# Kernel tuning notes

Hardware: AMD Instinct MI355X
Metric: run time of the kernel (lower is better)

Reference implementation:

```python
import jax, jax.numpy as jnp
import numpy as np

EPS = 1e-6


def _mp_match(reps, att, kernel):
    """BiMPM multi-perspective match.
    reps: (B,L,D); att: (B,L,D) or (B,1,D); kernel: (M,D).
    Returns (B,L,1+M): [tanh(sum(reps*att)), tanh(sum_d reps*kernel_m*att)].
    """
    prod = reps * att                                   # (B,L,D)
    cos = jnp.tanh(jnp.sum(prod, axis=-1, keepdims=True))   # (B,L,1)
    mp = jnp.tanh(jnp.einsum('bld,md->blm', prod, kernel))  # (B,L,M)
    return jnp.concatenate([cos, mp], axis=-1)


def setup_inputs() -> dict:
    key = jax.random.key(0)
    ks = jax.random.split(key, 12)
    B, Llt, Lrt, D, M, A = 32, 128, 128, 512, 64, 128
    H = D // 2
    u = lambda k, shape: jax.random.uniform(k, shape, jnp.float32, -0.05, 0.05)  # keras 'uniform' init
    return {
        'reps_lt': jax.random.normal(ks[0], (B, Llt, D), jnp.float32),
        'h_lt_fw': jax.random.normal(ks[1], (B, H), jnp.float32),
        'h_lt_bw': jax.random.normal(ks[2], (B, H), jnp.float32),
        'reps_rt': jax.random.normal(ks[3], (B, Lrt, D), jnp.float32),
        'h_rt_fw': jax.random.normal(ks[4], (B, H), jnp.float32),
        'h_rt_bw': jax.random.normal(ks[5], (B, H), jnp.float32),
        'kernel_full': u(ks[6], (M, D)),
        'kernel_mpool': u(ks[7], (M, D)),
        'attn_w1': u(ks[8], (D, A)),
        'diag_w': u(ks[9], (A,)),
        'kernel_att': u(ks[10], (M, D)),
        'kernel_maxatt': u(ks[11], (M, D)),
    }


def reference(reps_lt, h_lt_fw, h_lt_bw, reps_rt, h_rt_fw, h_rt_bw,
              kernel_full, kernel_mpool, attn_w1, diag_w,
              kernel_att, kernel_maxatt):
    # ---- full match: each left timestep vs last BiLSTM state of right ----
    h_rt = jnp.concatenate([h_rt_fw, h_rt_bw], axis=-1)[:, None, :]  # (B,1,D)
    full = _mp_match(reps_lt, h_rt, kernel_full)                     # (B,Ll,1+M)

    # ---- max-pooling match ----
    # t[b,r,l,m] = tanh(sum_d R[b,r,d]*K[m,d]*L[b,l,d]); max over right positions r
    r_scaled = jnp.einsum('brd,md->brmd', reps_rt, kernel_mpool)     # (B,Lr,M,D)
    t = jnp.tanh(jnp.einsum('brmd,bld->brlm', r_scaled, reps_lt))    # (B,Lr,Ll,M)
    mpool = jnp.max(t, axis=1)                                       # (B,Ll,M)

    # ---- attentive match ----
    a_lt = jnp.tanh(reps_lt @ attn_w1) * diag_w                      # (B,Ll,A)
    a_rt = jnp.tanh(reps_rt @ attn_w1)                               # (B,Lr,A)
    scores = jnp.einsum('bla,bra->blr', a_lt, a_rt)                  # (B,Ll,Lr)
    probs = jax.nn.softmax(scores, axis=-1)
    att = jnp.einsum('blr,brd->bld', probs, reps_rt)                 # (B,Ll,D)
    attentive = _mp_match(reps_lt, att, kernel_att)                  # (B,Ll,1+M)

    # ---- max-attentive match ----
    num = jnp.einsum('bld,brd->blr', reps_lt, reps_rt)
    n_lt = jnp.sqrt(jnp.maximum(jnp.sum(reps_lt * reps_lt, -1), EPS))[:, :, None]
    n_rt = jnp.sqrt(jnp.maximum(jnp.sum(reps_rt * reps_rt, -1), EPS))[:, None, :]
    rel = num / n_rt / n_lt                                          # (B,Ll,Lr)
    idx = jnp.argmax(rel, axis=2)                                    # (B,Ll) int
    max_att = jnp.take_along_axis(reps_rt, idx[:, :, None], axis=1)  # (B,Ll,D)
    maxatt = _mp_match(reps_lt, max_att, kernel_maxatt)              # (B,Ll,1+M)

    return jnp.concatenate([full, mpool, attentive, maxatt], axis=-1)  # (B,Ll,3+4M)
```

## Files before the change

kernel.cpp:

```cpp
#include <hip/hip_runtime.h>
#include <hip/hip_bf16.h>
#include <math.h>
#include <stdint.h>

typedef __attribute__((ext_vector_type(8))) short short8;
typedef __attribute__((ext_vector_type(4))) float float4v;

#define DEV static __device__ __forceinline__

DEV float bflo(unsigned int u) { union { unsigned int i; float f; } v; v.i = u << 16; return v.f; }
DEV float bfhi(unsigned int u) { union { unsigned int i; float f; } v; v.i = u & 0xffff0000u; return v.f; }
DEV unsigned short f2bf(float f) {
    union { float f; unsigned int i; } v; v.f = f;
    unsigned int x = v.i;
    return (unsigned short)((x + 0x7fffu + ((x >> 16) & 1u)) >> 16);
}
DEV unsigned int pack2(float a, float b) { return (unsigned int)f2bf(a) | ((unsigned int)f2bf(b) << 16); }
#if __has_builtin(__builtin_amdgcn_cvt_pk_bf16_f32)
DEV unsigned int pack2_fast(float a, float b) {
    typedef __attribute__((ext_vector_type(2))) short short2v;
    short2v r = __builtin_amdgcn_cvt_pk_bf16_f32(a, b);
    union { short2v s; unsigned int u; } v; v.s = r; return v.u;
}
#else
DEV unsigned int pack2_fast(float a, float b) { return pack2(a, b); }
#endif
DEV void unpack8(uint4 u, float* f) {
    f[0]=bflo(u.x); f[1]=bfhi(u.x); f[2]=bflo(u.y); f[3]=bfhi(u.y);
    f[4]=bflo(u.z); f[5]=bfhi(u.z); f[6]=bflo(u.w); f[7]=bfhi(u.w);
}

DEV void async16(const unsigned short* g, unsigned short* l) {
    __builtin_amdgcn_global_load_lds(
        (const __attribute__((address_space(1))) unsigned int*)g,
        (__attribute__((address_space(3))) unsigned int*)l, 16, 0, 0);
}

__global__ __launch_bounds__(256) void prep_kernel(const float* __restrict__ lt,
                                                   const float* __restrict__ rt,
                                                   const float* __restrict__ kf,
                                                   const float* __restrict__ kmp,
                                                   const float* __restrict__ ka,
                                                   const float* __restrict__ km,
                                                   const float* __restrict__ w1,
                                                   unsigned short* __restrict__ ltb,
                                                   unsigned short* __restrict__ rtb,
                                                   unsigned short* __restrict__ kb,
                                                   unsigned short* __restrict__ w1t,
                                                   unsigned short* __restrict__ rtbT,
                                                   double* __restrict__ rsq) {
    __shared__ double ws2[2][2];
    __shared__ float tile[32][33];
    int bid = blockIdx.x, t = threadIdx.x;
    if (bid < 1024) {
        bool isRt = bid >= 512;
        int base = (isRt ? (bid - 512) : bid) * 8;
        int rl = t >> 7;
        int c  = t & 127;
        const float* srcb = isRt ? rt : lt;
        unsigned short* dstb = isRt ? rtb : ltb;
        #pragma unroll
        for (int p = 0; p < 4; ++p) {
            int row = base + p * 2 + rl;
            const float* src = srcb + (size_t)row * 512;
            float4 v = *(const float4*)(src + c * 4);
            ushort4 o;
            o.x = f2bf(v.x); o.y = f2bf(v.y); o.z = f2bf(v.z); o.w = f2bf(v.w);
            *(ushort4*)(dstb + (size_t)row * 512 + c * 4) = o;
            if (isRt) {
                double s = (double)v.x * v.x + (double)v.y * v.y
                         + (double)v.z * v.z + (double)v.w * v.w;
                #pragma unroll
                for (int off = 1; off < 64; off <<= 1) s += __shfl_xor(s, off, 64);
                if ((c & 63) == 0) ws2[rl][c >> 6] = s;
                __syncthreads();
                if (c == 0) rsq[row] = 1.0 / sqrt(ws2[rl][0] + ws2[rl][1]);
                __syncthreads();
            }
        }
    } else if (bid < 1152) {
        int kbk = bid - 1024;
        int ksel = kbk >> 5;
        const float* src = (ksel == 0) ? kf : (ksel == 1) ? kmp : (ksel == 2) ? ka : km;
        int off = (kbk & 31) * 1024 + t * 4;
        float4 v = *(const float4*)(src + off);
        ushort4 o;
        o.x = f2bf(v.x); o.y = f2bf(v.y); o.z = f2bf(v.z); o.w = f2bf(v.w);
        *(ushort4*)(kb + ksel * 32768 + off) = o;
    } else if (bid < 1216) {
        int b2 = bid - 1152;
        int d0 = (b2 & 15) * 32, a0 = (b2 >> 4) * 32;
        int r = t >> 5, c = t & 31;
        #pragma unroll
        for (int i = 0; i < 32; i += 8)
            tile[r + i][c] = w1[(size_t)(d0 + r + i) * 128 + a0 + c];
        __syncthreads();
        #pragma unroll
        for (int i = 0; i < 32; i += 8)
            w1t[(size_t)(a0 + r + i) * 512 + d0 + c] = f2bf(tile[c][r + i]);
    } else {
        int b3 = bid - 1216;
        int b = b3 >> 6;
        int tid = b3 & 63;
        int d0 = (tid & 15) * 32;
        int r0 = (tid >> 4) * 32;
        int r = t >> 5, c = t & 31;
        #pragma unroll
        for (int i = 0; i < 32; i += 8)
            tile[r + i][c] = rt[(size_t)(b * 128 + r0 + r + i) * 512 + d0 + c];
        __syncthreads();
        #pragma unroll
        for (int i = 0; i < 32; i += 8)
            rtbT[(size_t)(b * 512 + d0 + r + i) * 128 + r0 + c] = f2bf(tile[c][r + i]);
    }
}

__global__ __launch_bounds__(256, 3) void uber_kernel(
        const unsigned short* __restrict__ ltb,
        const unsigned short* __restrict__ rtb,
        const unsigned short* __restrict__ kmb,
        const unsigned short* __restrict__ w1t,
        const float* __restrict__ diag,
        unsigned short* __restrict__ a_all,
        const double* __restrict__ rsq,
        unsigned int* __restrict__ candp,
        float* __restrict__ out) {
    __shared__ __align__(16) unsigned char smem[52224];
    int bx = blockIdx.x;
    int t = threadIdx.x;
    int wave = t >> 6, lane = t & 63;
    int q = lane >> 4, col = lane & 15, kq = q * 8;

    if (bx < 2048) {
        int xcd = bx & 7, jj = bx >> 3;
        int b = xcd * 4 + (jj >> 6);
        int m = jj & 63;
        unsigned short* ltS = (unsigned short*)smem;
        unsigned short* rtL = (unsigned short*)(smem + 16384);
        float (*mx)[2] = (float(*)[2])(smem + 16384 + 32768);
        int wl = wave & 1, wr = wave >> 1;
        const unsigned short* ltp = ltb + (size_t)b * 65536;
        const unsigned short* rtp = rtb + (size_t)b * 65536;
        const unsigned short* kr = kmb + (size_t)m * 512;
        int srow = t >> 3, cg8 = t & 7, cg = cg8 * 8;
        int gsw = (cg8 ^ (srow & 7)) * 8;
        int wbase = (t & ~63) * 8;

        #pragma unroll
        for (int it = 0; it < 4; ++it)
            async16(rtp + (size_t)(it * 32 + srow) * 512 + gsw,
                    rtL + it * 2048 + wbase);
        uint4 pk = *(const uint4*)(kr + cg);
        uint4 plt[4];
        #pragma unroll
        for (int it = 0; it < 4; ++it)
            plt[it] = *(const uint4*)(ltp + (size_t)(it * 32 + srow) * 512 + cg);

        float4v acc[4][4] = {};
        for (int k0i = 0; k0i < 8; ++k0i) {
            float kf8[8]; unpack8(pk, kf8);
            #pragma unroll
            for (int it = 0; it < 4; ++it) {
                int row = it * 32 + srow;
                float lf[8]; unpack8(plt[it], lf);
                uint4 s;
                s.x = pack2_fast(lf[0] * kf8[0], lf[1] * kf8[1]);
                s.y = pack2_fast(lf[2] * kf8[2], lf[3] * kf8[3]);
                s.z = pack2_fast(lf[4] * kf8[4], lf[5] * kf8[5]);
                s.w = pack2_fast(lf[6] * kf8[6], lf[7] * kf8[7]);
                *(uint4*)&ltS[row * 64 + gsw] = s;
            }
            __syncthreads();
            if (k0i < 7) {
                int k0n = (k0i + 1) * 64;
                int bofs = ((k0i + 1) & 1) * 8192;
                #pragma unroll
                for (int it = 0; it < 4; ++it)
                    async16(rtp + (size_t)(it * 32 + srow) * 512 + k0n + gsw,
                            rtL + bofs + it * 2048 + wbase);
                pk = *(const uint4*)(kr + k0n + cg);
                #pragma unroll
                for (int it = 0; it < 4; ++it)
                    plt[it] = *(const uint4*)(ltp + (size_t)(it * 32 + srow) * 512 + k0n + cg);
            }
            const unsigned short* rb = rtL + (k0i & 1) * 8192;
            #pragma unroll
            for (int kk = 0; kk < 64; kk += 32) {
                short8 af[4], bfr[4];
                #pragma unroll
                for (int i = 0; i < 4; ++i) {
                    int rowA = wl * 64 + i * 16 + col;
                    int slotA = ((kk >> 3) + q) ^ (rowA & 7);
                    af[i] = *(const short8*)&ltS[rowA * 64 + slotA * 8];
                }
                #pragma unroll
                for (int j = 0; j < 4; ++j) {
                    int row = wr * 64 + j * 16 + col;
                    int slot = ((kk >> 3) + q) ^ (row & 7);
                    bfr[j] = *(const short8*)&rb[row * 64 + slot * 8];
                }
                #pragma unroll
                for (int i = 0; i < 4; ++i)
                    #pragma unroll
                    for (int j = 0; j < 4; ++j)
                        acc[i][j] = __builtin_amdgcn_mfma_f32_16x16x32_bf16(af[i], bfr[j], acc[i][j], 0, 0, 0);
            }
            __syncthreads();
        }
        #pragma unroll
        for (int i = 0; i < 4; ++i)
            #pragma unroll
            for (int ii = 0; ii < 4; ++ii) {
                float v = fmaxf(fmaxf(acc[i][0][ii], acc[i][1][ii]), fmaxf(acc[i][2][ii], acc[i][3][ii]));
                #pragma unroll
                for (int off = 1; off < 16; off <<= 1) v = fmaxf(v, __shfl_xor(v, off, 64));
                if (col == 0) mx[wl * 64 + i * 16 + q * 4 + ii][wr] = v;
            }
        __syncthreads();
        if (t < 128)
            out[((size_t)(b * 128 + t)) * 259 + 65 + m] = tanhf(fmaxf(mx[t][0], mx[t][1]));

    } else if (bx < 2080) {
        int sb = bx - 2048;
        int xcd = sb & 7;
        int b = xcd * 4 + (sb >> 3);
        unsigned short* ltS = (unsigned short*)smem;
        unsigned short* rtL = (unsigned short*)(smem + 16384);
        float* rsqf = (float*)(smem + 49152);
        unsigned int (*candL)[2] = (unsigned int(*)[2])(smem + 49664);
        int wl = wave & 1, wr = wave >> 1;
        const unsigned short* ltp = ltb + (size_t)b * 65536;
        const unsigned short* rtp = rtb + (size_t)b * 65536;
        int srow = t >> 3, cg8 = t & 7, cg = cg8 * 8;
        int gsw = (cg8 ^ (srow & 7)) * 8;
        int wbase = (t & ~63) * 8;

        #pragma unroll
        for (int it = 0; it < 4; ++it)
            async16(rtp + (size_t)(it * 32 + srow) * 512 + gsw,
                    rtL + it * 2048 + wbase);
        uint4 plt[4];
        #pragma unroll
        for (int it = 0; it < 4; ++it)
            plt[it] = *(const uint4*)(ltp + (size_t)(it * 32 + srow) * 512 + cg);
        if (t < 128) rsqf[t] = (float)rsq[b * 128 + t];

        float4v acc[4][4] = {};
        for (int k0i = 0; k0i < 8; ++k0i) {
            #pragma unroll
            for (int it = 0; it < 4; ++it) {
                int row = it * 32 + srow;
                *(uint4*)&ltS[row * 64 + gsw] = plt[it];
            }
            __syncthreads();
            if (k0i < 7) {
                int k0n = (k0i + 1) * 64;
                int bofs = ((k0i + 1) & 1) * 8192;
                #pragma unroll
                for (int it = 0; it < 4; ++it)
                    async16(rtp + (size_t)(it * 32 + srow) * 512 + k0n + gsw,
                            rtL + bofs + it * 2048 + wbase);
                #pragma unroll
                for (int it = 0; it < 4; ++it)
                    plt[it] = *(const uint4*)(ltp + (size_t)(it * 32 + srow) * 512 + k0n + cg);
            }
            const unsigned short* rb = rtL + (k0i & 1) * 8192;
            #pragma unroll
            for (int kk = 0; kk < 64; kk += 32) {
                short8 af[4], bfr[4];
                #pragma unroll
                for (int i = 0; i < 4; ++i) {
                    int rowA = wl * 64 + i * 16 + col;
                    int slotA = ((kk >> 3) + q) ^ (rowA & 7);
                    af[i] = *(const short8*)&ltS[rowA * 64 + slotA * 8];
                }
                #pragma unroll
                for (int j = 0; j < 4; ++j) {
                    int row = wr * 64 + j * 16 + col;
                    int slot = ((kk >> 3) + q) ^ (row & 7);
                    bfr[j] = *(const short8*)&rb[row * 64 + slot * 8];
                }
                #pragma unroll
                for (int i = 0; i < 4; ++i)
                    #pragma unroll
                    for (int j = 0; j < 4; ++j)
                        acc[i][j] = __builtin_amdgcn_mfma_f32_16x16x32_bf16(af[i], bfr[j], acc[i][j], 0, 0, 0);
            }
            __syncthreads();
        }
        float rq[4];
        #pragma unroll
        for (int j = 0; j < 4; ++j) rq[j] = rsqf[wr * 64 + j * 16 + col];
        #pragma unroll
        for (int i = 0; i < 4; ++i)
            #pragma unroll
            for (int ii = 0; ii < 4; ++ii) {
                float v1 = -3.0e38f, v2 = -3.0e38f; int i1 = 0, i2 = 1;
                #pragma unroll
                for (int j = 0; j < 4; ++j) {
                    int rc = wr * 64 + j * 16 + col;
                    float s = acc[i][j][ii] * rq[j];
                    if (s > v1) { v2 = v1; i2 = i1; v1 = s; i1 = rc; }
                    else if (s > v2) { v2 = s; i2 = rc; }
                }
                #pragma unroll
                for (int off = 1; off < 16; off <<= 1) {
                    float u1 = __shfl_xor(v1, off, 64); int j1 = __shfl_xor(i1, off, 64);
                    float u2 = __shfl_xor(v2, off, 64); int j2 = __shfl_xor(i2, off, 64);
                    if (u1 > v1) {
                        float ov = v1; int oi = i1;
                        v1 = u1; i1 = j1;
                        if (u2 > ov) { v2 = u2; i2 = j2; } else { v2 = ov; i2 = oi; }
                    } else if (u1 > v2) { v2 = u1; i2 = j1; }
                }
                if (col == 0)
                    candL[wl * 64 + i * 16 + q * 4 + ii][wr] =
                        (unsigned int)i1 | ((unsigned int)i2 << 8);
            }
        __syncthreads();
        if (t < 128)
            candp[b * 128 + t] = candL[t][0] | (candL[t][1] << 16);

    } else {
        int R0 = (bx - 2080) * 32;
        unsigned short (*aS)[72] = (unsigned short(*)[72])smem;
        unsigned short (*bS)[72] = (unsigned short(*)[72])(smem + 4608);
        float* diagS = (float*)(smem + 4608 + 18432);
        int wl = wave & 1, wr = wave >> 1;
        if (t < 128) diagS[t] = diag[t];
        const unsigned short* src = (R0 < 4096) ? (ltb + (size_t)R0 * 512) : (rtb + (size_t)(R0 - 4096) * 512);
        float4v acc[4] = {};
        for (int k0 = 0; k0 < 512; k0 += 64) {
            {
                int row = t >> 3, cg = (t & 7) * 8;
                *(uint4*)&aS[row][cg] = *(const uint4*)(src + (size_t)row * 512 + k0 + cg);
            }
            #pragma unroll
            for (int it = 0; it < 4; ++it) {
                int id = it * 256 + t;
                int row = id >> 3, cg = (id & 7) * 8;
                *(uint4*)&bS[row][cg] = *(const uint4*)(w1t + (size_t)row * 512 + k0 + cg);
            }
            __syncthreads();
            #pragma unroll
            for (int kk = 0; kk < 64; kk += 32) {
                short8 af = *(const short8*)&aS[wl * 16 + col][kk + kq];
                #pragma unroll
                for (int j = 0; j < 4; ++j) {
                    short8 bf = *(const short8*)&bS[wr * 64 + j * 16 + col][kk + kq];
                    acc[j] = __builtin_amdgcn_mfma_f32_16x16x32_bf16(af, bf, acc[j], 0, 0, 0);
                }
            }
            __syncthreads();
        }
        bool isLt = (R0 < 4096);
        #pragma unroll
        for (int j = 0; j < 4; ++j)
            #pragma unroll
            for (int ii = 0; ii < 4; ++ii) {
                int rowl = wl * 16 + q * 4 + ii;
                int n = wr * 64 + j * 16 + col;
                float v = tanhf(acc[j][ii]);
                if (isLt) v *= diagS[n];
                a_all[((size_t)(R0 + rowl)) * 128 + n] = f2bf(v);
            }
    }
}

__global__ __launch_bounds__(512, 4) void tail_kernel(
        const unsigned short* __restrict__ a_all,
        const unsigned short* __restrict__ rtb,
        const unsigned short* __restrict__ rtbT,
        const float* __restrict__ ltf,
        const float* __restrict__ rtf,
        const double* __restrict__ rsq,
        const unsigned short* __restrict__ kb,
        const float* __restrict__ hfw,
        const float* __restrict__ hbw,
        const unsigned int* __restrict__ candp,
        float* __restrict__ out) {
    __shared__ __align__(16) unsigned char smem[81664];
    int bx = blockIdx.x;
    int t = threadIdx.x;
    int wave = t >> 6, lane = t & 63;
    int q = lane >> 4, col = lane & 15, kq = q * 8;

    if (bx < 256) {
        int b = bx & 31, lg = bx >> 5;
        int L0 = lg * 16;
        unsigned short (*altS)[136]  = (unsigned short(*)[136])(smem);
        unsigned short (*artS)[136]  = (unsigned short(*)[136])(smem + 4352);
        unsigned short (*prodsF)[520]= (unsigned short(*)[520])(smem + 55552);
        float (*pmax)[8] = (float(*)[8])(smem + 80640);
        float (*psum)[8] = (float(*)[8])(smem + 81152);
        const unsigned short* kb_att = kb + 2 * 32768;

        if (t < 256) {
            int row = t >> 4, c0 = (t & 15) * 8;
            *(uint4*)&altS[row][c0] = *(const uint4*)(a_all + ((size_t)(b * 128 + L0 + row)) * 128 + c0);
        }
        {
            int row = t >> 2, c0 = (t & 3) * 32;
            const unsigned short* src = a_all + ((size_t)(4096 + b * 128 + row)) * 128 + c0;
            #pragma unroll
            for (int i = 0; i < 4; ++i)
                *(uint4*)&artS[row][c0 + i * 8] = *(const uint4*)(src + i * 8);
        }
        __syncthreads();

        float4v acc = {};
        #pragma unroll
        for (int kk = 0; kk < 128; kk += 32) {
            short8 af = *(const short8*)&altS[col][kk + kq];
            short8 bf = *(const short8*)&artS[wave * 16 + col][kk + kq];
            acc = __builtin_amdgcn_mfma_f32_16x16x32_bf16(af, bf, acc, 0, 0, 0);
        }
        float m4[4], p4[4];
        #pragma unroll
        for (int ii = 0; ii < 4; ++ii) {
            float v = acc[ii];
            #pragma unroll
            for (int off = 1; off < 16; off <<= 1) v = fmaxf(v, __shfl_xor(v, off, 64));
            m4[ii] = v;
        }
        if (col == 0) {
            #pragma unroll
            for (int ii = 0; ii < 4; ++ii) pmax[q * 4 + ii][wave] = m4[ii];
        }
        __syncthreads();
        #pragma unroll
        for (int ii = 0; ii < 4; ++ii) {
            float M = pmax[q * 4 + ii][0];
            #pragma unroll
            for (int w = 1; w < 8; ++w) M = fmaxf(M, pmax[q * 4 + ii][w]);
            p4[ii] = expf(acc[ii] - M);
            float s = p4[ii];
            #pragma unroll
            for (int off = 1; off < 16; off <<= 1) s += __shfl_xor(s, off, 64);
            m4[ii] = s;
        }
        if (col == 0) {
            #pragma unroll
            for (int ii = 0; ii < 4; ++ii) psum[q * 4 + ii][wave] = m4[ii];
        }
        __syncthreads();
        unsigned short* Pb = (unsigned short*)smem;
        #pragma unroll
        for (int ii = 0; ii < 4; ++ii) {
            float S = psum[q * 4 + ii][0] + psum[q * 4 + ii][1] + psum[q * 4 + ii][2] + psum[q * 4 + ii][3]
                    + psum[q * 4 + ii][4] + psum[q * 4 + ii][5] + psum[q * 4 + ii][6] + psum[q * 4 + ii][7];
            Pb[(q * 4 + ii) * 136 + wave * 16 + col] = f2bf(p4[ii] / S);
        }

        unsigned short* Bc = (unsigned short*)(smem + 4352);
        float* attF = (float*)(smem + 39168);
        const unsigned short* rtT = rtbT + (size_t)b * 65536;
        for (int cc = 0; cc < 4; ++cc) {
            #pragma unroll
            for (int i = 0; i < 4; ++i) {
                int rid = i * 32 + (t >> 4);
                int d   = (rid >> 4) * 64 + cc * 16 + (rid & 15);
                int sg  = (t & 15) ^ (rid & 15);
                async16(rtT + (size_t)d * 128 + sg * 8, Bc + i * 4096 + t * 8);
            }
            __syncthreads();
            float4v pacc = {};
            #pragma unroll
            for (int ks = 0; ks < 4; ++ks) {
                short8 afP = *(const short8*)&Pb[col * 136 + ks * 32 + kq];
                short8 bfB = *(const short8*)&Bc[(wave * 16 + col) * 128 + (((ks * 4 + q) ^ col) * 8)];
                pacc = __builtin_amdgcn_mfma_f32_16x16x32_bf16(afP, bfB, pacc, 0, 0, 0);
            }
            #pragma unroll
            for (int ii = 0; ii < 4; ++ii)
                attF[(q * 4 + ii) * 512 + wave * 64 + cc * 16 + col] = pacc[ii];
            __syncthreads();
        }

        int l = t >> 5, cd = t & 31;
        float a8[2][8];
        #pragma unroll
        for (int pass = 0; pass < 2; ++pass) {
            *(float4*)&a8[pass][0] = *(const float4*)&attF[l * 512 + pass * 256 + cd * 8];
            *(float4*)&a8[pass][4] = *(const float4*)&attF[l * 512 + pass * 256 + cd * 8 + 4];
        }
        __syncthreads();

        int grow = b * 128 + L0 + l;
        const float* ltrow = ltf + (size_t)grow * 512;
        float csum = 0.f;
        #pragma unroll
        for (int pass = 0; pass < 2; ++pass) {
            int d0 = pass * 256 + cd * 8;
            float lf[8];
            *(float4*)&lf[0] = *(const float4*)(ltrow + d0);
            *(float4*)&lf[4] = *(const float4*)(ltrow + d0 + 4);
            float pf[8];
            #pragma unroll
            for (int k = 0; k < 8; ++k) { pf[k] = lf[k] * a8[pass][k]; csum += pf[k]; }
            uint4 o;
            o.x = pack2(pf[0], pf[1]); o.y = pack2(pf[2], pf[3]);
            o.z = pack2(pf[4], pf[5]); o.w = pack2(pf[6], pf[7]);
            *(uint4*)&prodsF[l][d0] = o;
        }
        #pragma unroll
        for (int off = 1; off < 32; off <<= 1) csum += __shfl_xor(csum, off, 64);
        if (cd == 0) out[(size_t)grow * 259 + 129] = tanhf(csum);

        unsigned short* Ks = &artS[0][0];
        float* red = (float*)(smem + 39168);
        for (int half = 0; half < 2; ++half) {
            __syncthreads();
            {
                int row = t >> 4, c0 = (t & 15) * 32;
                const unsigned short* src = kb_att + ((size_t)(half * 32 + row)) * 512 + c0;
                #pragma unroll
                for (int i = 0; i < 4; ++i)
                    *(uint4*)&Ks[row * 520 + c0 + i * 8] = *(const uint4*)(src + i * 8);
            }
            __syncthreads();
            float4v pacc[2] = {};
            #pragma unroll
            for (int kk = 0; kk < 64; kk += 32) {
                short8 af = *(const short8*)&prodsF[col][wave * 64 + kk + kq];
                #pragma unroll
                for (int j = 0; j < 2; ++j) {
                    short8 bf = *(const short8*)&Ks[(j * 16 + col) * 520 + wave * 64 + kk + kq];
                    pacc[j] = __builtin_amdgcn_mfma_f32_16x16x32_bf16(af, bf, pacc[j], 0, 0, 0);
                }
            }
            #pragma unroll
            for (int j = 0; j < 2; ++j)
                #pragma unroll
                for (int ii = 0; ii < 4; ++ii)
                    red[((wave * 2 + j) * 16 + q * 4 + ii) * 16 + col] = pacc[j][ii];
            __syncthreads();
            {
                int ll = t >> 5, jm = t & 31;
                int j = jm >> 4, mc = jm & 15;
                float s = 0.f;
                #pragma unroll
                for (int w = 0; w < 8; ++w) s += red[((w * 2 + j) * 16 + ll) * 16 + mc];
                out[((size_t)(b * 128 + L0 + ll)) * 259 + 130 + half * 32 + jm] = tanhf(s);
            }
        }

    } else {
        int idB = bx - 256;
        int lg = idB & 7, b = (idB >> 3) & 31;
        int mode = (idB >> 8) ? 2 : 0;
        int L0 = lg * 16;
        unsigned short (*prods)[520] = (unsigned short(*)[520])smem;
        unsigned short* Ks = (unsigned short*)(smem + 16640);
        float* red = (float*)(smem + 49920);
        double* dvs2 = (double*)(smem + 66304);
        int* idxl = (int*)(smem + 66816);
        const unsigned short* Kp = kb + (size_t)((mode == 0) ? 0 : 3 * 32768);
        int obase = (mode == 0) ? 0 : 194;

        if (mode == 2) {
            int dotid = t >> 3, sub = t & 7;
            int l = dotid >> 2, c = dotid & 3;
            unsigned int cpl = candp[b * 128 + L0 + l];
            int r = (cpl >> (c * 8)) & 0xff;
            const float* lrow = ltf + ((size_t)(b * 128 + L0 + l)) * 512;
            const float* rrow = rtf + ((size_t)(b * 128 + r)) * 512;
            double s = 0.0;
            #pragma unroll 8
            for (int k = 0; k < 64; ++k) {
                int d = sub * 64 + k;
                s = fma((double)lrow[d], (double)rrow[d], s);
            }
            #pragma unroll
            for (int off = 1; off < 8; off <<= 1) s += __shfl_xor(s, off, 64);
            if (sub == 0) dvs2[dotid] = s * rsq[b * 128 + r];
            __syncthreads();
            if (t < 16) {
                unsigned int cl = candp[b * 128 + L0 + t];
                int bi = 256; double bv = -1.0e300;
                #pragma unroll
                for (int cc = 0; cc < 4; ++cc) {
                    int rr = (cl >> (cc * 8)) & 0xff;
                    double v = dvs2[t * 4 + cc];
                    if (v > bv || (v == bv && rr < bi)) { bv = v; bi = rr; }
                }
                idxl[t] = bi;
            }
            __syncthreads();
        }

        if (t < 256) {
            int l = t >> 4, c = t & 15;
            int grow = b * 128 + L0 + l;
            const float* ltrow = ltf + (size_t)grow * 512;
            const unsigned short* avrow = 0;
            if (mode == 2) avrow = rtb + ((size_t)(b * 128 + idxl[l])) * 512;
            float csum = 0.f;
            #pragma unroll
            for (int pass = 0; pass < 4; ++pass) {
                int d0 = pass * 128 + c * 8;
                float lf[8], af[8], pf[8];
                *(float4*)&lf[0] = *(const float4*)(ltrow + d0);
                *(float4*)&lf[4] = *(const float4*)(ltrow + d0 + 4);
                if (mode == 0) {
                    const float* h = (d0 < 256) ? (hfw + b * 256 + d0) : (hbw + b * 256 + d0 - 256);
                    *(float4*)&af[0] = *(const float4*)h;
                    *(float4*)&af[4] = *(const float4*)(h + 4);
                } else {
                    uint4 av = *(const uint4*)(avrow + d0);
                    unpack8(av, af);
                }
                #pragma unroll
                for (int k = 0; k < 8; ++k) { pf[k] = lf[k] * af[k]; csum += pf[k]; }
                uint4 o;
                o.x = pack2(pf[0], pf[1]); o.y = pack2(pf[2], pf[3]);
                o.z = pack2(pf[4], pf[5]); o.w = pack2(pf[6], pf[7]);
                *(uint4*)&prods[l][d0] = o;
            }
            #pragma unroll
            for (int off = 1; off < 16; off <<= 1) csum += __shfl_xor(csum, off, 64);
            if (c == 0) out[(size_t)grow * 259 + obase] = tanhf(csum);
        }
        for (int half = 0; half < 2; ++half) {
            {
                int row = t >> 4, c0 = (t & 15) * 32;
                const unsigned short* src = Kp + ((size_t)(half * 32 + row)) * 512 + c0;
                #pragma unroll
                for (int i = 0; i < 4; ++i)
                    *(uint4*)&Ks[row * 520 + c0 + i * 8] = *(const uint4*)(src + i * 8);
            }
            __syncthreads();
            float4v acc2[2] = {};
            #pragma unroll
            for (int kk = 0; kk < 64; kk += 32) {
                short8 af = *(const short8*)&prods[col][wave * 64 + kk + kq];
                #pragma unroll
                for (int j = 0; j < 2; ++j) {
                    short8 bf = *(const short8*)&Ks[(j * 16 + col) * 520 + wave * 64 + kk + kq];
                    acc2[j] = __builtin_amdgcn_mfma_f32_16x16x32_bf16(af, bf, acc2[j], 0, 0, 0);
                }
            }
            #pragma unroll
            for (int j = 0; j < 2; ++j)
                #pragma unroll
                for (int ii = 0; ii < 4; ++ii)
                    red[((wave * 2 + j) * 16 + q * 4 + ii) * 16 + col] = acc2[j][ii];
            __syncthreads();
            {
                int ll = t >> 5, jm = t & 31;
                int j = jm >> 4, mc = jm & 15;
                float s = 0.f;
                #pragma unroll
                for (int w = 0; w < 8; ++w) s += red[((w * 2 + j) * 16 + ll) * 16 + mc];
                out[((size_t)(b * 128 + L0 + ll)) * 259 + obase + 1 + half * 32 + jm] = tanhf(s);
            }
            __syncthreads();
        }
    }
}

extern "C" void kernel_launch(void* const* d_in, const int* in_sizes, int n_in,
                              void* d_out, int out_size, void* d_ws, size_t ws_size,
                              hipStream_t stream) {
    const float* lt  = (const float*)d_in[0];
    const float* rt  = (const float*)d_in[3];
    const float* hfw = (const float*)d_in[4];
    const float* hbw = (const float*)d_in[5];
    const float* kf  = (const float*)d_in[6];
    const float* kmp = (const float*)d_in[7];
    const float* w1  = (const float*)d_in[8];
    const float* dia = (const float*)d_in[9];
    const float* ka  = (const float*)d_in[10];
    const float* km  = (const float*)d_in[11];
    float* out = (float*)d_out;

    char* wsb = (char*)d_ws;
    unsigned short* ltb16 = (unsigned short*)(wsb);
    unsigned short* rtb16 = (unsigned short*)(wsb + 4194304);
    unsigned short* kb16  = (unsigned short*)(wsb + 8388608);
    unsigned short* w1t   = (unsigned short*)(wsb + 8650752);
    unsigned short* a_all = (unsigned short*)(wsb + 8781824);
    unsigned short* rtbT  = (unsigned short*)(wsb + 10878976);
    double*         rsq   = (double*)(wsb + 15073280);
    unsigned int*   candp = (unsigned int*)(wsb + 15106048);

    prep_kernel<<<3264, 256, 0, stream>>>(lt, rt, kf, kmp, ka, km, w1, ltb16, rtb16, kb16, w1t, rtbT, rsq);
    uber_kernel<<<2336, 256, 0, stream>>>(ltb16, rtb16, kb16 + 32768, w1t, dia, a_all,
                                          rsq, candp, out);
    tail_kernel<<<768, 512, 0, stream>>>(a_all, rtb16, rtbT, lt, rt, rsq, kb16, hfw, hbw, candp, out);
}
```

Measured before the change: 176.9 us.

## Move max-pool GEMM into final kernel, interleaved with attentive and max-att blocks

The max-pooling match blocks (2048 of them) move out of the middle kernel into the final kernel, which now uses 512 threads so each block has 8 waves splitting the right-side rows. Block indices are interleaved per XCD so that mpool, attentive and max-attentive work share one launch. The middle kernel keeps only candidate selection and the attention projections. The goal is to overlap the heavy mpool GEMM with the latency-bound tail work and shorten the middle launch. In exchange, each mpool block now does a 4-way cross-wave max reduction through shared memory, and the larger blocks may lower occupancy.

```diff
diff --git a/kernel.cpp b/kernel.cpp
--- a/kernel.cpp
+++ b/kernel.cpp
@@ -115,113 +115,22 @@
     }
 }
 
-__global__ __launch_bounds__(256, 3) void uber_kernel(
+__global__ __launch_bounds__(256, 3) void mid_kernel(
         const unsigned short* __restrict__ ltb,
         const unsigned short* __restrict__ rtb,
-        const unsigned short* __restrict__ kmb,
         const unsigned short* __restrict__ w1t,
         const float* __restrict__ diag,
         unsigned short* __restrict__ a_all,
         const double* __restrict__ rsq,
-        unsigned int* __restrict__ candp,
-        float* __restrict__ out) {
+        unsigned int* __restrict__ candp) {
     __shared__ __align__(16) unsigned char smem[52224];
     int bx = blockIdx.x;
     int t = threadIdx.x;
     int wave = t >> 6, lane = t & 63;
     int q = lane >> 4, col = lane & 15, kq = q * 8;
 
-    if (bx < 2048) {
-        int xcd = bx & 7, jj = bx >> 3;
-        int b = xcd * 4 + (jj >> 6);
-        int m = jj & 63;
-        unsigned short* ltS = (unsigned short*)smem;
-        unsigned short* rtL = (unsigned short*)(smem + 16384);
-        float (*mx)[2] = (float(*)[2])(smem + 16384 + 32768);
-        int wl = wave & 1, wr = wave >> 1;
-        const unsigned short* ltp = ltb + (size_t)b * 65536;
-        const unsigned short* rtp = rtb + (size_t)b * 65536;
-        const unsigned short* kr = kmb + (size_t)m * 512;
-        int srow = t >> 3, cg8 = t & 7, cg = cg8 * 8;
-        int gsw = (cg8 ^ (srow & 7)) * 8;
-        int wbase = (t & ~63) * 8;
-
-        #pragma unroll
-        for (int it = 0; it < 4; ++it)
-            async16(rtp + (size_t)(it * 32 + srow) * 512 + gsw,
-                    rtL + it * 2048 + wbase);
-        uint4 pk = *(const uint4*)(kr + cg);
-        uint4 plt[4];
-        #pragma unroll
-        for (int it = 0; it < 4; ++it)
-            plt[it] = *(const uint4*)(ltp + (size_t)(it * 32 + srow) * 512 + cg);
-
-        float4v acc[4][4] = {};
-        for (int k0i = 0; k0i < 8; ++k0i) {
-            float kf8[8]; unpack8(pk, kf8);
-            #pragma unroll
-            for (int it = 0; it < 4; ++it) {
-                int row = it * 32 + srow;
-                float lf[8]; unpack8(plt[it], lf);
-                uint4 s;
-                s.x = pack2_fast(lf[0] * kf8[0], lf[1] * kf8[1]);
-                s.y = pack2_fast(lf[2] * kf8[2], lf[3] * kf8[3]);
-                s.z = pack2_fast(lf[4] * kf8[4], lf[5] * kf8[5]);
-                s.w = pack2_fast(lf[6] * kf8[6], lf[7] * kf8[7]);
-                *(uint4*)&ltS[row * 64 + gsw] = s;
-            }
-            __syncthreads();
-            if (k0i < 7) {
-                int k0n = (k0i + 1) * 64;
-                int bofs = ((k0i + 1) & 1) * 8192;
-                #pragma unroll
-                for (int it = 0; it < 4; ++it)
-                    async16(rtp + (size_t)(it * 32 + srow) * 512 + k0n + gsw,
-                            rtL + bofs + it * 2048 + wbase);
-                pk = *(const uint4*)(kr + k0n + cg);
-                #pragma unroll
-                for (int it = 0; it < 4; ++it)
-                    plt[it] = *(const uint4*)(ltp + (size_t)(it * 32 + srow) * 512 + k0n + cg);
-            }
-            const unsigned short* rb = rtL + (k0i & 1) * 8192;
-            #pragma unroll
-            for (int kk = 0; kk < 64; kk += 32) {
-                short8 af[4], bfr[4];
-                #pragma unroll
-                for (int i = 0; i < 4; ++i) {
-                    int rowA = wl * 64 + i * 16 + col;
-                    int slotA = ((kk >> 3) + q) ^ (rowA & 7);
-                    af[i] = *(const short8*)&ltS[rowA * 64 + slotA * 8];
-                }
-                #pragma unroll
-                for (int j = 0; j < 4; ++j) {
-                    int row = wr * 64 + j * 16 + col;
-                    int slot = ((kk >> 3) + q) ^ (row & 7);
-                    bfr[j] = *(const short8*)&rb[row * 64 + slot * 8];
-                }
-                #pragma unroll
-                for (int i = 0; i < 4; ++i)
-                    #pragma unroll
-                    for (int j = 0; j < 4; ++j)
-                        acc[i][j] = __builtin_amdgcn_mfma_f32_16x16x32_bf16(af[i], bfr[j], acc[i][j], 0, 0, 0);
-            }
-            __syncthreads();
-        }
-        #pragma unroll
-        for (int i = 0; i < 4; ++i)
-            #pragma unroll
-            for (int ii = 0; ii < 4; ++ii) {
-                float v = fmaxf(fmaxf(acc[i][0][ii], acc[i][1][ii]), fmaxf(acc[i][2][ii], acc[i][3][ii]));
-                #pragma unroll
-                for (int off = 1; off < 16; off <<= 1) v = fmaxf(v, __shfl_xor(v, off, 64));
-                if (col == 0) mx[wl * 64 + i * 16 + q * 4 + ii][wr] = v;
-            }
-        __syncthreads();
-        if (t < 128)
-            out[((size_t)(b * 128 + t)) * 259 + 65 + m] = tanhf(fmaxf(mx[t][0], mx[t][1]));
-
-    } else if (bx < 2080) {
-        int sb = bx - 2048;
+    if (bx < 32) {
+        int sb = bx;
         int xcd = sb & 7;
         int b = xcd * 4 + (sb >> 3);
         unsigned short* ltS = (unsigned short*)smem;
@@ -322,7 +231,7 @@
             candp[b * 128 + t] = candL[t][0] | (candL[t][1] << 16);
 
     } else {
-        int R0 = (bx - 2080) * 32;
+        int R0 = (bx - 32) * 32;
         unsigned short (*aS)[72] = (unsigned short(*)[72])smem;
         unsigned short (*bS)[72] = (unsigned short(*)[72])(smem + 4608);
         float* diagS = (float*)(smem + 4608 + 18432);
@@ -367,9 +276,11 @@
     }
 }
 
-__global__ __launch_bounds__(512, 4) void tail_kernel(
+__global__ __launch_bounds__(512, 4) void main_kernel(
+        const unsigned short* __restrict__ ltb,
+        const unsigned short* __restrict__ rtb,
+        const unsigned short* __restrict__ kmb,
         const unsigned short* __restrict__ a_all,
-        const unsigned short* __restrict__ rtb,
         const unsigned short* __restrict__ rtbT,
         const float* __restrict__ ltf,
         const float* __restrict__ rtf,
@@ -385,8 +296,105 @@
     int wave = t >> 6, lane = t & 63;
     int q = lane >> 4, col = lane & 15, kq = q * 8;
 
-    if (bx < 256) {
-        int b = bx & 31, lg = bx >> 5;
+    int xcd = bx & 7;
+    int s = bx >> 3;
+    int g = s / 11;
+    int r = s - g * 11;
+
+    if (r < 8) {
+        int lm = g * 8 + r;
+        int b = xcd * 4 + (lm >> 6);
+        int m = lm & 63;
+        unsigned short* ltS = (unsigned short*)smem;
+        unsigned short* rtL = (unsigned short*)(smem + 16384);
+        float (*mx)[4] = (float(*)[4])(smem + 49152);
+        int wl = wave & 1, wr = wave >> 1;
+        const unsigned short* ltp = ltb + (size_t)b * 65536;
+        const unsigned short* rtp = rtb + (size_t)b * 65536;
+        const unsigned short* kr = kmb + (size_t)m * 512;
+        int srow = t >> 3, cg8 = t & 7, cg = cg8 * 8;
+        int gsw = (cg8 ^ (srow & 7)) * 8;
+
+        #pragma unroll
+        for (int it = 0; it < 2; ++it)
+            async16(rtp + (size_t)(it * 64 + srow) * 512 + gsw,
+                    rtL + it * 4096 + t * 8);
+        uint4 pk = *(const uint4*)(kr + cg);
+        uint4 plt[2];
+        #pragma unroll
+        for (int it = 0; it < 2; ++it)
+            plt[it] = *(const uint4*)(ltp + (size_t)(it * 64 + srow) * 512 + cg);
+
+        float4v acc[4][2] = {};
+        for (int k0i = 0; k0i < 8; ++k0i) {
+            float kf8[8]; unpack8(pk, kf8);
+            #pragma unroll
+            for (int it = 0; it < 2; ++it) {
+                int row = it * 64 + srow;
+                float lf[8]; unpack8(plt[it], lf);
+                uint4 sv;
+                sv.x = pack2_fast(lf[0] * kf8[0], lf[1] * kf8[1]);
+                sv.y = pack2_fast(lf[2] * kf8[2], lf[3] * kf8[3]);
+                sv.z = pack2_fast(lf[4] * kf8[4], lf[5] * kf8[5]);
+                sv.w = pack2_fast(lf[6] * kf8[6], lf[7] * kf8[7]);
+                *(uint4*)&ltS[row * 64 + gsw] = sv;
+            }
+            __syncthreads();
+            if (k0i < 7) {
+                int k0n = (k0i + 1) * 64;
+                int bofs = ((k0i + 1) & 1) * 8192;
+                #pragma unroll
+                for (int it = 0; it < 2; ++it)
+                    async16(rtp + (size_t)(it * 64 + srow) * 512 + k0n + gsw,
+                            rtL + bofs + it * 4096 + t * 8);
+                pk = *(const uint4*)(kr + k0n + cg);
+                #pragma unroll
+                for (int it = 0; it < 2; ++it)
+                    plt[it] = *(const uint4*)(ltp + (size_t)(it * 64 + srow) * 512 + k0n + cg);
+            }
+            const unsigned short* rb = rtL + (k0i & 1) * 8192;
+            #pragma unroll
+            for (int kk = 0; kk < 64; kk += 32) {
+                short8 af[4], bfr[2];
+                #pragma unroll
+                for (int i = 0; i < 4; ++i) {
+                    int rowA = wl * 64 + i * 16 + col;
+                    int slotA = ((kk >> 3) + q) ^ (rowA & 7);
+                    af[i] = *(const short8*)&ltS[rowA * 64 + slotA * 8];
+                }
+                #pragma unroll
+                for (int j = 0; j < 2; ++j) {
+                    int row = wr * 32 + j * 16 + col;
+                    int slot = ((kk >> 3) + q) ^ (row & 7);
+                    bfr[j] = *(const short8*)&rb[row * 64 + slot * 8];
+                }
+                #pragma unroll
+                for (int i = 0; i < 4; ++i)
+                    #pragma unroll
+                    for (int j = 0; j < 2; ++j)
+                        acc[i][j] = __builtin_amdgcn_mfma_f32_16x16x32_bf16(af[i], bfr[j], acc[i][j], 0, 0, 0);
+            }
+            __syncthreads();
+        }
+        #pragma unroll
+        for (int i = 0; i < 4; ++i)
+            #pragma unroll
+            for (int ii = 0; ii < 4; ++ii) {
+                float v = fmaxf(acc[i][0][ii], acc[i][1][ii]);
+                #pragma unroll
+                for (int off = 1; off < 16; off <<= 1) v = fmaxf(v, __shfl_xor(v, off, 64));
+                if (col == 0) mx[wl * 64 + i * 16 + q * 4 + ii][wr] = v;
+            }
+        __syncthreads();
+        if (t < 128) {
+            float v = fmaxf(fmaxf(mx[t][0], mx[t][1]), fmaxf(mx[t][2], mx[t][3]));
+            out[((size_t)(b * 128 + t)) * 259 + 65 + m] = tanhf(v);
+        }
+
+    } else if (r == 8) {
+        int la = g;
+        int b = xcd * 4 + (la >> 3);
+        int lg = la & 7;
         int L0 = lg * 16;
         unsigned short (*altS)[136]  = (unsigned short(*)[136])(smem);
         unsigned short (*artS)[136]  = (unsigned short(*)[136])(smem + 4352);
@@ -434,10 +442,10 @@
             #pragma unroll
             for (int w = 1; w < 8; ++w) M = fmaxf(M, pmax[q * 4 + ii][w]);
             p4[ii] = expf(acc[ii] - M);
-            float s = p4[ii];
-            #pragma unroll
-            for (int off = 1; off < 16; off <<= 1) s += __shfl_xor(s, off, 64);
-            m4[ii] = s;
+            float sv = p4[ii];
+            #pragma unroll
+            for (int off = 1; off < 16; off <<= 1) sv += __shfl_xor(sv, off, 64);
+            m4[ii] = sv;
         }
         if (col == 0) {
             #pragma unroll
@@ -538,17 +546,18 @@
             {
                 int ll = t >> 5, jm = t & 31;
                 int j = jm >> 4, mc = jm & 15;
-                float s = 0.f;
-                #pragma unroll
-                for (int w = 0; w < 8; ++w) s += red[((w * 2 + j) * 16 + ll) * 16 + mc];
-                out[((size_t)(b * 128 + L0 + ll)) * 259 + 130 + half * 32 + jm] = tanhf(s);
+                float sv = 0.f;
+                #pragma unroll
+                for (int w = 0; w < 8; ++w) sv += red[((w * 2 + j) * 16 + ll) * 16 + mc];
+                out[((size_t)(b * 128 + L0 + ll)) * 259 + 130 + half * 32 + jm] = tanhf(sv);
             }
         }
 
     } else {
-        int idB = bx - 256;
-        int lg = idB & 7, b = (idB >> 3) & 31;
-        int mode = (idB >> 8) ? 2 : 0;
+        int lb = g * 2 + (r - 9);
+        int mode = (lb >> 5) ? 2 : 0;
+        int b = xcd * 4 + ((lb >> 3) & 3);
+        int lg = lb & 7;
         int L0 = lg * 16;
         unsigned short (*prods)[520] = (unsigned short(*)[520])smem;
         unsigned short* Ks = (unsigned short*)(smem + 16640);
@@ -562,18 +571,18 @@
             int dotid = t >> 3, sub = t & 7;
             int l = dotid >> 2, c = dotid & 3;
             unsigned int cpl = candp[b * 128 + L0 + l];
-            int r = (cpl >> (c * 8)) & 0xff;
+            int rr0 = (cpl >> (c * 8)) & 0xff;
             const float* lrow = ltf + ((size_t)(b * 128 + L0 + l)) * 512;
-            const float* rrow = rtf + ((size_t)(b * 128 + r)) * 512;
-            double s = 0.0;
+            const float* rrow = rtf + ((size_t)(b * 128 + rr0)) * 512;
+            double sv = 0.0;
             #pragma unroll 8
             for (int k = 0; k < 64; ++k) {
                 int d = sub * 64 + k;
-                s = fma((double)lrow[d], (double)rrow[d], s);
-            }
-            #pragma unroll
-            for (int off = 1; off < 8; off <<= 1) s += __shfl_xor(s, off, 64);
-            if (sub == 0) dvs2[dotid] = s * rsq[b * 128 + r];
+                sv = fma((double)lrow[d], (double)rrow[d], sv);
+            }
+            #pragma unroll
+            for (int off = 1; off < 8; off <<= 1) sv += __shfl_xor(sv, off, 64);
+            if (sub == 0) dvs2[dotid] = sv * rsq[b * 128 + rr0];
             __syncthreads();
             if (t < 16) {
                 unsigned int cl = candp[b * 128 + L0 + t];
@@ -649,10 +658,10 @@
             {
                 int ll = t >> 5, jm = t & 31;
                 int j = jm >> 4, mc = jm & 15;
-                float s = 0.f;
-                #pragma unroll
-                for (int w = 0; w < 8; ++w) s += red[((w * 2 + j) * 16 + ll) * 16 + mc];
-                out[((size_t)(b * 128 + L0 + ll)) * 259 + obase + 1 + half * 32 + jm] = tanhf(s);
+                float sv = 0.f;
+                #pragma unroll
+                for (int w = 0; w < 8; ++w) sv += red[((w * 2 + j) * 16 + ll) * 16 + mc];
+                out[((size_t)(b * 128 + L0 + ll)) * 259 + obase + 1 + half * 32 + jm] = tanhf(sv);
             }
             __syncthreads();
         }
@@ -685,7 +694,7 @@
     unsigned int*   candp = (unsigned int*)(wsb + 15106048);
 
     prep_kernel<<<3264, 256, 0, stream>>>(lt, rt, kf, kmp, ka, km, w1, ltb16, rtb16, kb16, w1t, rtbT, rsq);
-    uber_kernel<<<2336, 256, 0, stream>>>(ltb16, rtb16, kb16 + 32768, w1t, dia, a_all,
-                                          rsq, candp, out);
-    tail_kernel<<<768, 512, 0, stream>>>(a_all, rtb16, rtbT, lt, rt, rsq, kb16, hfw, hbw, candp, out);
+    mid_kernel<<<288, 256, 0, stream>>>(ltb16, rtb16, w1t, dia, a_all, rsq, candp);
+    main_kernel<<<2816, 512, 0, stream>>>(ltb16, rtb16, kb16 + 32768, a_all, rtbT,
+                                          lt, rt, rsq, kb16, hfw, hbw, candp, out);
 }
```

Result: slower. 198.8 us (+12.4%).

## Shrink tail_kernel shared memory by aliasing buffers to raise occupancy

Applied to the files above, without the earlier changes.

Cuts tail_kernel's static shared memory from about 80KB to about 52KB. It does this by splitting the attention-times-rt B staging into two half-K chunks and by aliasing the prods, Ks and red buffers onto regions that are no longer live. Launch bounds rise from 4 to 6 blocks per CU, so more 512-thread blocks can be resident at once. In exchange it adds extra barriers (per half-chunk and around the reduction buffer reuse), which could offset the occupancy gain.

```diff
diff --git a/kernel.cpp b/kernel.cpp
--- a/kernel.cpp
+++ b/kernel.cpp
@@ -367,7 +367,7 @@
     }
 }
 
-__global__ __launch_bounds__(512, 4) void tail_kernel(
+__global__ __launch_bounds__(512, 6) void tail_kernel(
         const unsigned short* __restrict__ a_all,
         const unsigned short* __restrict__ rtb,
         const unsigned short* __restrict__ rtbT,
@@ -379,7 +379,7 @@
         const float* __restrict__ hbw,
         const unsigned int* __restrict__ candp,
         float* __restrict__ out) {
-    __shared__ __align__(16) unsigned char smem[81664];
+    __shared__ __align__(16) unsigned char smem[53504];
     int bx = blockIdx.x;
     int t = threadIdx.x;
     int wave = t >> 6, lane = t & 63;
@@ -390,9 +390,8 @@
         int L0 = lg * 16;
         unsigned short (*altS)[136]  = (unsigned short(*)[136])(smem);
         unsigned short (*artS)[136]  = (unsigned short(*)[136])(smem + 4352);
-        unsigned short (*prodsF)[520]= (unsigned short(*)[520])(smem + 55552);
-        float (*pmax)[8] = (float(*)[8])(smem + 80640);
-        float (*psum)[8] = (float(*)[8])(smem + 81152);
+        float (*pmax)[8] = (float(*)[8])(smem + 39168);
+        float (*psum)[8] = (float(*)[8])(smem + 39680);
         const unsigned short* kb_att = kb + 2 * 32768;
 
         if (t < 256) {
@@ -434,10 +433,10 @@
             #pragma unroll
             for (int w = 1; w < 8; ++w) M = fmaxf(M, pmax[q * 4 + ii][w]);
             p4[ii] = expf(acc[ii] - M);
-            float s = p4[ii];
-            #pragma unroll
-            for (int off = 1; off < 16; off <<= 1) s += __shfl_xor(s, off, 64);
-            m4[ii] = s;
+            float sv = p4[ii];
+            #pragma unroll
+            for (int off = 1; off < 16; off <<= 1) sv += __shfl_xor(sv, off, 64);
+            m4[ii] = sv;
         }
         if (col == 0) {
             #pragma unroll
@@ -453,29 +452,35 @@
         }
 
         unsigned short* Bc = (unsigned short*)(smem + 4352);
-        float* attF = (float*)(smem + 39168);
+        float* attF = (float*)(smem + 20736);
         const unsigned short* rtT = rtbT + (size_t)b * 65536;
         for (int cc = 0; cc < 4; ++cc) {
-            #pragma unroll
-            for (int i = 0; i < 4; ++i) {
-                int rid = i * 32 + (t >> 4);
-                int d   = (rid >> 4) * 64 + cc * 16 + (rid & 15);
-                int sg  = (t & 15) ^ (rid & 15);
-                async16(rtT + (size_t)d * 128 + sg * 8, Bc + i * 4096 + t * 8);
-            }
-            __syncthreads();
             float4v pacc = {};
-            #pragma unroll
-            for (int ks = 0; ks < 4; ++ks) {
-                short8 afP = *(const short8*)&Pb[col * 136 + ks * 32 + kq];
-                short8 bfB = *(const short8*)&Bc[(wave * 16 + col) * 128 + (((ks * 4 + q) ^ col) * 8)];
-                pacc = __builtin_amdgcn_mfma_f32_16x16x32_bf16(afP, bfB, pacc, 0, 0, 0);
+            for (int rh = 0; rh < 2; ++rh) {
+                #pragma unroll
+                for (int k = 0; k < 2; ++k) {
+                    int id = (k * 8 + wave) * 64 + lane;
+                    int row = id >> 3, grp = id & 7;
+                    int d   = (row >> 4) * 64 + cc * 16 + (row & 15);
+                    int sg  = grp ^ (row & 7);
+                    async16(rtT + (size_t)d * 128 + rh * 64 + sg * 8,
+                            Bc + (size_t)id * 8);
+                }
+                __syncthreads();
+                #pragma unroll
+                for (int ks = 0; ks < 2; ++ks) {
+                    short8 afP = *(const short8*)&Pb[col * 136 + rh * 64 + ks * 32 + kq];
+                    int rowB = wave * 16 + col;
+                    short8 bfB = *(const short8*)&Bc[rowB * 64 + (((ks * 4 + q) ^ (rowB & 7)) * 8)];
+                    pacc = __builtin_amdgcn_mfma_f32_16x16x32_bf16(afP, bfB, pacc, 0, 0, 0);
+                }
+                __syncthreads();
             }
             #pragma unroll
             for (int ii = 0; ii < 4; ++ii)
                 attF[(q * 4 + ii) * 512 + wave * 64 + cc * 16 + col] = pacc[ii];
-            __syncthreads();
-        }
+        }
+        __syncthreads();
 
         int l = t >> 5, cd = t & 31;
         float a8[2][8];
@@ -485,6 +490,10 @@
             *(float4*)&a8[pass][4] = *(const float4*)&attF[l * 512 + pass * 256 + cd * 8 + 4];
         }
         __syncthreads();
+
+        unsigned short (*prodsF)[520] = (unsigned short(*)[520])smem;
+        unsigned short* Ks = (unsigned short*)(smem + 16640);
+        float* red = (float*)(smem + 16640);
 
         int grow = b * 128 + L0 + l;
         const float* ltrow = ltf + (size_t)grow * 512;
@@ -507,8 +516,6 @@
         for (int off = 1; off < 32; off <<= 1) csum += __shfl_xor(csum, off, 64);
         if (cd == 0) out[(size_t)grow * 259 + 129] = tanhf(csum);
 
-        unsigned short* Ks = &artS[0][0];
-        float* red = (float*)(smem + 39168);
         for (int half = 0; half < 2; ++half) {
             __syncthreads();
             {
@@ -529,6 +536,7 @@
                     pacc[j] = __builtin_amdgcn_mfma_f32_16x16x32_bf16(af, bf, pacc[j], 0, 0, 0);
                 }
             }
+            __syncthreads();
             #pragma unroll
             for (int j = 0; j < 2; ++j)
                 #pragma unroll
@@ -538,10 +546,10 @@
             {
                 int ll = t >> 5, jm = t & 31;
                 int j = jm >> 4, mc = jm & 15;
-                float s = 0.f;
-                #pragma unroll
-                for (int w = 0; w < 8; ++w) s += red[((w * 2 + j) * 16 + ll) * 16 + mc];
-                out[((size_t)(b * 128 + L0 + ll)) * 259 + 130 + half * 32 + jm] = tanhf(s);
+                float sv = 0.f;
+                #pragma unroll
+                for (int w = 0; w < 8; ++w) sv += red[((w * 2 + j) * 16 + ll) * 16 + mc];
+                out[((size_t)(b * 128 + L0 + ll)) * 259 + 130 + half * 32 + jm] = tanhf(sv);
             }
         }
 
@@ -552,9 +560,9 @@
         int L0 = lg * 16;
         unsigned short (*prods)[520] = (unsigned short(*)[520])smem;
         unsigned short* Ks = (unsigned short*)(smem + 16640);
-        float* red = (float*)(smem + 49920);
-        double* dvs2 = (double*)(smem + 66304);
-        int* idxl = (int*)(smem + 66816);
+        float* red = (float*)(smem + 16640);
+        double* dvs2 = (double*)(smem + 49920);
+        int* idxl = (int*)(smem + 50432);
         const unsigned short* Kp = kb + (size_t)((mode == 0) ? 0 : 3 * 32768);
         int obase = (mode == 0) ? 0 : 194;
 
@@ -562,18 +570,18 @@
             int dotid = t >> 3, sub = t & 7;
             int l = dotid >> 2, c = dotid & 3;
             unsigned int cpl = candp[b * 128 + L0 + l];
-            int r = (cpl >> (c * 8)) & 0xff;
+            int rr0 = (cpl >> (c * 8)) & 0xff;
             const float* lrow = ltf + ((size_t)(b * 128 + L0 + l)) * 512;
-            const float* rrow = rtf + ((size_t)(b * 128 + r)) * 512;
-            double s = 0.0;
+            const float* rrow = rtf + ((size_t)(b * 128 + rr0)) * 512;
+            double sv = 0.0;
             #pragma unroll 8
             for (int k = 0; k < 64; ++k) {
                 int d = sub * 64 + k;
-                s = fma((double)lrow[d], (double)rrow[d], s);
-            }
-            #pragma unroll
-            for (int off = 1; off < 8; off <<= 1) s += __shfl_xor(s, off, 64);
-            if (sub == 0) dvs2[dotid] = s * rsq[b * 128 + r];
+                sv = fma((double)lrow[d], (double)rrow[d], sv);
+            }
+            #pragma unroll
+            for (int off = 1; off < 8; off <<= 1) sv += __shfl_xor(sv, off, 64);
+            if (sub == 0) dvs2[dotid] = sv * rsq[b * 128 + rr0];
             __syncthreads();
             if (t < 16) {
                 unsigned int cl = candp[b * 128 + L0 + t];
@@ -622,6 +630,7 @@
             if (c == 0) out[(size_t)grow * 259 + obase] = tanhf(csum);
         }
         for (int half = 0; half < 2; ++half) {
+            if (half == 1) __syncthreads();
             {
                 int row = t >> 4, c0 = (t & 15) * 32;
                 const unsigned short* src = Kp + ((size_t)(half * 32 + row)) * 512 + c0;
@@ -640,6 +649,7 @@
                     acc2[j] = __builtin_amdgcn_mfma_f32_16x16x32_bf16(af, bf, acc2[j], 0, 0, 0);
                 }
             }
+            __syncthreads();
             #pragma unroll
             for (int j = 0; j < 2; ++j)
                 #pragma unroll
@@ -649,12 +659,11 @@
             {
                 int ll = t >> 5, jm = t & 31;
                 int j = jm >> 4, mc = jm & 15;
-                float s = 0.f;
-                #pragma unroll
-                for (int w = 0; w < 8; ++w) s += red[((w * 2 + j) * 16 + ll) * 16 + mc];
-                out[((size_t)(b * 128 + L0 + ll)) * 259 + obase + 1 + half * 32 + jm] = tanhf(s);
-            }
-            __syncthreads();
+                float sv = 0.f;
+                #pragma unroll
+                for (int w = 0; w < 8; ++w) sv += red[((w * 2 + j) * 16 + ll) * 16 + mc];
+                out[((size_t)(b * 128 + L0 + ll)) * 259 + obase + 1 + half * 32 + jm] = tanhf(sv);
+            }
         }
     }
 }
```

Result: no change. 175.7 us, median of 2 (-0.7%).
